# Optimization experiments

Measured on AMD Instinct MI355X. Metric: run time of the kernel, lower is better.

## Reference

```python
import jax, jax.numpy as jnp
import numpy as np

N = 100000
E = 1600000
C_IN = 128
C_OUT = 128
EPS = 1e-5


def setup_inputs() -> dict:
    key = jax.random.key(0)
    ks = jax.random.split(key, 8)
    x = jax.random.normal(ks[0], (N, C_IN), dtype=jnp.float32)
    edge_index = jax.random.randint(ks[1], (2, E), 0, N, dtype=jnp.int64)
    s_proj = 1.0 / np.sqrt(C_IN)
    s_out = 1.0 / np.sqrt(C_IN)
    W_proj = jax.random.uniform(ks[2], (C_IN, C_IN), jnp.float32, -s_proj, s_proj)
    b_proj = jax.random.uniform(ks[3], (C_IN,), jnp.float32, -s_proj, s_proj)
    W_l = jax.random.uniform(ks[4], (C_OUT, C_IN), jnp.float32, -s_out, s_out)
    b_l = jax.random.uniform(ks[5], (C_OUT,), jnp.float32, -s_out, s_out)
    W_r = jax.random.uniform(ks[6], (C_OUT, C_IN), jnp.float32, -s_out, s_out)
    gamma = jnp.ones((C_OUT,), jnp.float32)
    beta = jnp.zeros((C_OUT,), jnp.float32)
    return {"x": x, "edge_index": edge_index, "W_proj": W_proj, "b_proj": b_proj,
            "W_l": W_l, "b_l": b_l, "W_r": W_r, "gamma": gamma, "beta": beta}


def reference(x, edge_index, W_proj, b_proj, W_l, b_l, W_r, gamma, beta):
    # SAGEConv(project=True, aggr='sum'): project+ReLU source features per node,
    # gather along edges, scatter-sum at targets, then lin_l(agg) + lin_r(x_root).
    src, dst = edge_index[0], edge_index[1]
    h = jax.nn.relu(x @ W_proj.T + b_proj)            # [N, C_IN]
    msg = h[src]                                       # [E, C_IN] edge gather
    agg = jax.ops.segment_sum(msg, dst, num_segments=N)  # [N, C_IN]
    out = agg @ W_l.T + b_l + x @ W_r.T                # [N, C_OUT] (root uses unprojected x)
    # LayerNorm(c_out)
    mu = jnp.mean(out, axis=-1, keepdims=True)
    var = jnp.var(out, axis=-1, keepdims=True)
    return (out - mu) * jax.lax.rsqrt(var + EPS) * gamma + beta
```

## Files before the change

kernel.cpp:

```cpp
#include <hip/hip_runtime.h>
#include <stdint.h>

#define NN 100000
#define NE 1600000
#define C  128
#define NB 782
#define CAP 4096
#define SB_SHIFT 13
#define MB 782
#define P1B 250

typedef __attribute__((ext_vector_type(8))) short short8;
typedef __attribute__((ext_vector_type(4))) float f32x4;

__device__ __forceinline__ float bf2f(uint16_t u) {
  union { uint32_t u; float f; } v; v.u = ((uint32_t)u) << 16; return v.f;
}
__device__ __forceinline__ uint16_t f2bf(float f) {
  union { float f; uint32_t u; } v; v.f = f;
  uint32_t r = v.u + 0x7fffu + ((v.u >> 16) & 1u);
  return (uint16_t)(r >> 16);
}
__device__ __forceinline__ float2 bf2x2(uint32_t u) {
  return make_float2(bf2f((uint16_t)u), bf2f((uint16_t)(u >> 16)));
}

__global__ __launch_bounds__(256) void cast3_k(
    const float* __restrict__ a, const float* __restrict__ b, const float* __restrict__ c,
    uint16_t* __restrict__ oa, uint16_t* __restrict__ ob, uint16_t* __restrict__ oc)
{
  int i = blockIdx.x * 256 + threadIdx.x;
  int which = i >> 12, j = i & 4095;
  const float* s = which == 0 ? a : (which == 1 ? b : c);
  uint16_t* d    = which == 0 ? oa : (which == 1 ? ob : oc);
  float4 v = ((const float4*)s)[j];
  uint2 p;
  p.x = (uint32_t)f2bf(v.x) | ((uint32_t)f2bf(v.y) << 16);
  p.y = (uint32_t)f2bf(v.z) | ((uint32_t)f2bf(v.w) << 16);
  ((uint2*)d)[j] = p;
}


__global__ __launch_bounds__(512) void fused_front_k(
    const float* __restrict__ x, const uint16_t* __restrict__ wpb,
    const uint16_t* __restrict__ wrb,
    const float* __restrict__ bp, const float* __restrict__ bl,
    uint16_t* __restrict__ h, uint16_t* __restrict__ rb,
    const int* __restrict__ esrc, const int* __restrict__ edst,
    int* __restrict__ gcnt, uint32_t* __restrict__ ebuf)
{
  extern __shared__ uint8_t slds[];
  const int t = threadIdx.x;

  if (blockIdx.x < MB) {
#pragma unroll
    for (int qq = 0; qq < 4; ++qq) {
      int ci = qq * 512 + t;
      int c = ci >> 4, k16 = ci & 15;
      int slot = (k16 ^ (c & 15)) << 4;
      *(short8*)(slds + c * 256 + slot)         = *(const short8*)(wpb + ci * 8);
      *(short8*)(slds + 32768 + c * 256 + slot) = *(const short8*)(wrb + ci * 8);
    }
    __syncthreads();

    const int w = t >> 6, lane = t & 63;
    const int tile_m = blockIdx.x * 128 + w * 16;
    if (tile_m >= NN) return;
    const int r16 = lane & 15, g = lane >> 4;

    int arow = tile_m + r16; if (arow >= NN) arow = NN - 1;
    short8 a[4];
    const float* xp = x + (size_t)arow * C + g * 8;
#pragma unroll
    for (int kk = 0; kk < 4; ++kk) {
      float4 u = *(const float4*)(xp + kk * 32);
      float4 v = *(const float4*)(xp + kk * 32 + 4);
      short8 av;
      av[0] = (short)f2bf(u.x); av[1] = (short)f2bf(u.y);
      av[2] = (short)f2bf(u.z); av[3] = (short)f2bf(u.w);
      av[4] = (short)f2bf(v.x); av[5] = (short)f2bf(v.y);
      av[6] = (short)f2bf(v.z); av[7] = (short)f2bf(v.w);
      a[kk] = av;
    }

#pragma unroll
    for (int nt = 0; nt < 8; ++nt) {
      f32x4 ap = {0.f, 0.f, 0.f, 0.f};
      f32x4 ar = {0.f, 0.f, 0.f, 0.f};
      const int c = nt * 16 + r16;
      const uint8_t* rbp = slds + c * 256;
      const uint8_t* rbr = slds + 32768 + c * 256;
#pragma unroll
      for (int kk = 0; kk < 4; ++kk) {
        int slot = (((kk << 2) + g) ^ (c & 15)) << 4;
        ap = __builtin_amdgcn_mfma_f32_16x16x32_bf16(a[kk], *(const short8*)(rbp + slot), ap, 0, 0, 0);
        ar = __builtin_amdgcn_mfma_f32_16x16x32_bf16(a[kk], *(const short8*)(rbr + slot), ar, 0, 0, 0);
      }
      const float bpv = bp[c], blv = bl[c];
#pragma unroll
      for (int rr = 0; rr < 4; ++rr) {
        int row = tile_m + g * 4 + rr;
        if (row < NN) {
          float vh = ap[rr] + bpv;
          vh = vh > 0.f ? vh : 0.f;
          h[(size_t)row * C + c]  = f2bf(vh);
          rb[(size_t)row * C + c] = f2bf(ar[rr] + blv);
        }
      }
    }
  } else {
    int* bh = (int*)slds;
    int* gb = bh + NB;
    const int blk = blockIdx.x - MB;
    const int base = blk * 6400;

    for (int i = t; i < NB; i += 512) bh[i] = 0;

    const int4* ed4 = (const int4*)(edst + base);
    const int4* es4 = (const int4*)(esrc + base);
    int4 dv[4], sv[4];
    bool val[4];
#pragma unroll
    for (int k = 0; k < 4; ++k) {
      int i = t + k * 512;
      val[k] = (i < 1600);
      if (val[k]) { dv[k] = ed4[i]; sv[k] = es4[i]; }
    }
    __syncthreads();

#pragma unroll
    for (int k = 0; k < 4; ++k) if (val[k]) {
      atomicAdd(&bh[dv[k].x >> 7], 1); atomicAdd(&bh[dv[k].y >> 7], 1);
      atomicAdd(&bh[dv[k].z >> 7], 1); atomicAdd(&bh[dv[k].w >> 7], 1);
    }
    __syncthreads();

    for (int i = t; i < NB; i += 512) {
      int c = bh[i];
      gb[i] = c ? atomicAdd(&gcnt[i], c) : 0;
      bh[i] = 0;
    }
    __syncthreads();

#define P1_SCATTER(d, s) do { \
      int bb = (d) >> 7; \
      int o = atomicAdd(&bh[bb], 1); \
      int pos = gb[bb] + o; \
      if (pos < CAP) ebuf[(size_t)bb * CAP + pos] = ((uint32_t)((d) & 127) << 17) | (uint32_t)(s); \
    } while (0)

#pragma unroll
    for (int k = 0; k < 4; ++k) if (val[k]) {
      P1_SCATTER(dv[k].x, sv[k].x); P1_SCATTER(dv[k].y, sv[k].y);
      P1_SCATTER(dv[k].z, sv[k].z); P1_SCATTER(dv[k].w, sv[k].w);
    }
#undef P1_SCATTER
  }
}

__global__ __launch_bounds__(256) void phase2_k(
    const uint32_t* __restrict__ ebuf, const int* __restrict__ gcnt,
    int* __restrict__ ssrc, int2* __restrict__ sdeg)
{
  __shared__ uint32_t raw[CAP];
  __shared__ int lout[CAP];
  __shared__ int cnt2[128 * 16];
  __shared__ int nd[128];
  __shared__ int psum[256];
  const int b = blockIdx.x, t = threadIdx.x;
  const int n0 = b * 128;

  int acc = 0;
  for (int i = t; i < b; i += 256) acc += gcnt[i];
  psum[t] = acc;
  __syncthreads();
  for (int off = 128; off > 0; off >>= 1) {
    if (t < off) psum[t] += psum[t + off];
    __syncthreads();
  }
  const int base = psum[0];
  int cnt = gcnt[b]; if (cnt > CAP) cnt = CAP;

  for (int i = t; i < 128 * 16; i += 256) cnt2[i] = 0;
  __syncthreads();
  for (int i = t; i < cnt; i += 256) {
    uint32_t v = ebuf[(size_t)b * CAP + i];
    raw[i] = v;
    atomicAdd(&cnt2[(v >> 17) * 16 + ((v & 0x1FFFFu) >> SB_SHIFT)], 1);
  }
  __syncthreads();

  int deg_t = 0;
  if (t < 128) {
#pragma unroll
    for (int i = 0; i < 16; ++i) deg_t += cnt2[t * 16 + i];
    nd[t] = deg_t;
  }
  __syncthreads();
  for (int off = 1; off < 128; off <<= 1) {
    int v = 0;
    if (t < 128 && t >= off) v = nd[t - off];
    __syncthreads();
    if (t < 128) nd[t] += v;
    __syncthreads();
  }
  if (t < 128) {
    int pref = nd[t] - deg_t;
    if (n0 + t < NN) sdeg[n0 + t] = make_int2(base + pref, deg_t);
    int run = pref;
#pragma unroll
    for (int i = 0; i < 16; ++i) { int c = cnt2[t * 16 + i]; cnt2[t * 16 + i] = run; run += c; }
  }
  __syncthreads();
  for (int i = t; i < cnt; i += 256) {
    uint32_t v = raw[i];
    int o = atomicAdd(&cnt2[(v >> 17) * 16 + ((v & 0x1FFFFu) >> SB_SHIFT)], 1);
    lout[o] = (int)(v & 0x1FFFFu);
  }
  __syncthreads();
  for (int i = t; i < cnt; i += 256) ssrc[base + i] = lout[i];
}

__global__ __launch_bounds__(256) void aggregate_k(
    const uint16_t* __restrict__ h, const int* __restrict__ ssrc,
    const int2* __restrict__ sdeg, uint16_t* __restrict__ agg)
{
  const int wid = (blockIdx.x * 256 + threadIdx.x) >> 6;
  if (wid >= NN) return;
  const int lane = threadIdx.x & 63;
  const int q = lane >> 4;
  const int l16 = lane & 15;
  const int2 sd = sdeg[wid];
  const int s0 = sd.x, cnt = sd.y;
  const size_t choff = (size_t)l16 * 8;
  float2 a0 = {0.f, 0.f}, a1 = {0.f, 0.f}, a2 = {0.f, 0.f}, a3 = {0.f, 0.f};

#define ACC8(v) do { \
    a0 += bf2x2((v).x); a1 += bf2x2((v).y); \
    a2 += bf2x2((v).z); a3 += bf2x2((v).w); \
  } while (0)

  if (cnt > 0) {
    int e0 = ssrc[s0 + ((q      < cnt) ? q      : cnt - 1)];
    int e1 = ssrc[s0 + ((q + 4  < cnt) ? q + 4  : cnt - 1)];
    int e2 = ssrc[s0 + ((q + 8  < cnt) ? q + 8  : cnt - 1)];
    int e3 = ssrc[s0 + ((q + 12 < cnt) ? q + 12 : cnt - 1)];
    for (int j = 0; j < cnt; j += 16) {
      uint4 v0 = *(const uint4*)(h + (size_t)e0 * C + choff);
      uint4 v1 = *(const uint4*)(h + (size_t)e1 * C + choff);
      uint4 v2 = *(const uint4*)(h + (size_t)e2 * C + choff);
      uint4 v3 = *(const uint4*)(h + (size_t)e3 * C + choff);
      const int jn = j + 16;
      if (jn < cnt) {
        e0 = ssrc[s0 + ((jn + q      < cnt) ? jn + q      : cnt - 1)];
        e1 = ssrc[s0 + ((jn + q + 4  < cnt) ? jn + q + 4  : cnt - 1)];
        e2 = ssrc[s0 + ((jn + q + 8  < cnt) ? jn + q + 8  : cnt - 1)];
        e3 = ssrc[s0 + ((jn + q + 12 < cnt) ? jn + q + 12 : cnt - 1)];
      }
      if (j + q      < cnt) ACC8(v0);
      if (j + q + 4  < cnt) ACC8(v1);
      if (j + q + 8  < cnt) ACC8(v2);
      if (j + q + 12 < cnt) ACC8(v3);
    }
  }
#undef ACC8

#pragma unroll
  for (int msk = 16; msk <= 32; msk <<= 1) {
    a0.x += __shfl_xor(a0.x, msk, 64); a0.y += __shfl_xor(a0.y, msk, 64);
    a1.x += __shfl_xor(a1.x, msk, 64); a1.y += __shfl_xor(a1.y, msk, 64);
    a2.x += __shfl_xor(a2.x, msk, 64); a2.y += __shfl_xor(a2.y, msk, 64);
    a3.x += __shfl_xor(a3.x, msk, 64); a3.y += __shfl_xor(a3.y, msk, 64);
  }
  if (q == 0) {
    uint4 p;
    p.x = (uint32_t)f2bf(a0.x) | ((uint32_t)f2bf(a0.y) << 16);
    p.y = (uint32_t)f2bf(a1.x) | ((uint32_t)f2bf(a1.y) << 16);
    p.z = (uint32_t)f2bf(a2.x) | ((uint32_t)f2bf(a2.y) << 16);
    p.w = (uint32_t)f2bf(a3.x) | ((uint32_t)f2bf(a3.y) << 16);
    *(uint4*)(agg + (size_t)wid * C + choff) = p;
  }
}

__global__ __launch_bounds__(512) void gemm_out_k(
    const uint16_t* __restrict__ aggb, const uint16_t* __restrict__ rb,
    const uint16_t* __restrict__ wlb, const float* __restrict__ gamma,
    const float* __restrict__ beta, float* __restrict__ out)
{
  __shared__ uint8_t wl[32768];
  const int t = threadIdx.x;
#pragma unroll
  for (int qq = 0; qq < 4; ++qq) {
    int ci = qq * 512 + t;
    int c = ci >> 4, k16 = ci & 15;
    *(short8*)(wl + c * 256 + ((k16 ^ (c & 15)) << 4)) = *(const short8*)(wlb + ci * 8);
  }
  __syncthreads();

  const int w = t >> 6, lane = t & 63;
  const int tile_m = blockIdx.x * 128 + w * 16;
  if (tile_m >= NN) return;
  const int r16 = lane & 15, g = lane >> 4;

  int arow = tile_m + r16; if (arow >= NN) arow = NN - 1;
  short8 a0[4];
  const uint16_t* p0 = aggb + (size_t)arow * C + g * 8;
#pragma unroll
  for (int kk = 0; kk < 4; ++kk) a0[kk] = *(const short8*)(p0 + kk * 32);

  f32x4 acc[8];
#pragma unroll
  for (int nt = 0; nt < 8; ++nt) {
    f32x4 c4 = {0.f, 0.f, 0.f, 0.f};
    const int c = nt * 16 + r16;
    const uint8_t* rbl = wl + c * 256;
#pragma unroll
    for (int kk = 0; kk < 4; ++kk) {
      short8 b = *(const short8*)(rbl + ((((kk << 2) + g) ^ (c & 15)) << 4));
      c4 = __builtin_amdgcn_mfma_f32_16x16x32_bf16(a0[kk], b, c4, 0, 0, 0);
    }
#pragma unroll
    for (int rr = 0; rr < 4; ++rr) {
      int row = tile_m + g * 4 + rr;
      int crow = row < NN ? row : NN - 1;
      c4[rr] += bf2f(rb[(size_t)crow * C + c]);
    }
    acc[nt] = c4;
  }

  float s1[4], s2[4];
#pragma unroll
  for (int rr = 0; rr < 4; ++rr) { s1[rr] = 0.f; s2[rr] = 0.f; }
#pragma unroll
  for (int nt = 0; nt < 8; ++nt)
#pragma unroll
    for (int rr = 0; rr < 4; ++rr) { float v = acc[nt][rr]; s1[rr] += v; s2[rr] += v * v; }
#pragma unroll
  for (int msk = 1; msk <= 8; msk <<= 1) {
#pragma unroll
    for (int rr = 0; rr < 4; ++rr) {
      s1[rr] += __shfl_xor(s1[rr], msk, 64);
      s2[rr] += __shfl_xor(s2[rr], msk, 64);
    }
  }
  float mean[4], rstd[4];
#pragma unroll
  for (int rr = 0; rr < 4; ++rr) {
    mean[rr] = s1[rr] * (1.f / C);
    float var = s2[rr] * (1.f / C) - mean[rr] * mean[rr];
    rstd[rr] = rsqrtf(var + 1e-5f);
  }
#pragma unroll
  for (int nt = 0; nt < 8; ++nt) {
    const int col = nt * 16 + r16;
    const float gmv = gamma[col], btv = beta[col];
#pragma unroll
    for (int rr = 0; rr < 4; ++rr) {
      int row = tile_m + g * 4 + rr;
      if (row < NN)
        out[(size_t)row * C + col] = (acc[nt][rr] - mean[rr]) * rstd[rr] * gmv + btv;
    }
  }
}

extern "C" void kernel_launch(void* const* d_in, const int* in_sizes, int n_in,
                              void* d_out, int out_size, void* d_ws, size_t ws_size,
                              hipStream_t stream)
{
  const float* x        = (const float*)d_in[0];
  const int* ei         = (const int*)d_in[1];
  const float* Wp       = (const float*)d_in[2];
  const float* bp       = (const float*)d_in[3];
  const float* Wl       = (const float*)d_in[4];
  const float* bl       = (const float*)d_in[5];
  const float* Wr       = (const float*)d_in[6];
  const float* gamma    = (const float*)d_in[7];
  const float* beta     = (const float*)d_in[8];
  float* out            = (float*)d_out;

  char* ws = (char*)d_ws;
  uint16_t* rb   = (uint16_t*)(ws + 0);
  uint16_t* h    = (uint16_t*)(ws + 25600000);
  uint32_t* ebuf = (uint32_t*)(ws + 51200000);
  uint16_t* aggb = (uint16_t*)(ws + 51200000);
  uint16_t* wpb  = (uint16_t*)(ws + 76800000);
  uint16_t* wlb  = (uint16_t*)(ws + 76832768);
  uint16_t* wrb  = (uint16_t*)(ws + 76865536);
  int2* sdeg     = (int2*)(ws + 76898304);
  int* gcnt      = (int*)(ws + 77698304);
  int* ssrc      = (int*)(ws + 78102400);

  const int* esrc = ei;
  const int* edst = ei + NE;

  hipMemsetAsync(gcnt, 0, NB * sizeof(int), stream);

  cast3_k<<<48, 256, 0, stream>>>(Wp, Wl, Wr, wpb, wlb, wrb);

  fused_front_k<<<MB + P1B, 512, 65536, stream>>>(
      x, wpb, wrb, bp, bl, h, rb, esrc, edst, gcnt, ebuf);

  phase2_k<<<NB, 256, 0, stream>>>(ebuf, gcnt, ssrc, sdeg);

  aggregate_k<<<(NN + 3) / 4, 256, 0, stream>>>(h, ssrc, sdeg, aggb);

  gemm_out_k<<<MB, 512, 0, stream>>>(aggb, rb, wlb, gamma, beta, out);
}
```

Before: 141.1 us.

## Transpose MFMA operands for row-contiguous vector stores and double front-kernel block size

Both GEMM kernels swap the MFMA A/B operands so each lane holds four consecutive columns of one row. This turns scattered 2-byte stores and loads of h, rb and out into packed uint2/float4 row-contiguous accesses and makes the LayerNorm reduction a two-step shuffle across lane groups. The fused front kernel also moves to 1024-thread blocks, with half as many GEMM and edge-binning blocks each covering twice the work, which halves the per-block weight staging into LDS. The cost is lower occupancy per block and more work per edge-binning block.

```diff
diff --git a/kernel.cpp b/kernel.cpp
--- a/kernel.cpp
+++ b/kernel.cpp
@@ -7,8 +7,9 @@
 #define NB 782
 #define CAP 4096
 #define SB_SHIFT 13
-#define MB 782
-#define P1B 250
+#define MBF 391
+#define P1B 125
+#define MBO 782
 
 typedef __attribute__((ext_vector_type(8))) short short8;
 typedef __attribute__((ext_vector_type(4))) float f32x4;
@@ -41,7 +42,7 @@
 }
 
 
-__global__ __launch_bounds__(512) void fused_front_k(
+__global__ __launch_bounds__(1024) void fused_front_k(
     const float* __restrict__ x, const uint16_t* __restrict__ wpb,
     const uint16_t* __restrict__ wrb,
     const float* __restrict__ bp, const float* __restrict__ bl,
@@ -52,10 +53,10 @@
   extern __shared__ uint8_t slds[];
   const int t = threadIdx.x;
 
-  if (blockIdx.x < MB) {
-#pragma unroll
-    for (int qq = 0; qq < 4; ++qq) {
-      int ci = qq * 512 + t;
+  if (blockIdx.x < MBF) {
+#pragma unroll
+    for (int qq = 0; qq < 2; ++qq) {
+      int ci = qq * 1024 + t;
       int c = ci >> 4, k16 = ci & 15;
       int slot = (k16 ^ (c & 15)) << 4;
       *(short8*)(slds + c * 256 + slot)         = *(const short8*)(wpb + ci * 8);
@@ -64,11 +65,12 @@
     __syncthreads();
 
     const int w = t >> 6, lane = t & 63;
-    const int tile_m = blockIdx.x * 128 + w * 16;
+    const int tile_m = blockIdx.x * 256 + w * 16;
     if (tile_m >= NN) return;
     const int r16 = lane & 15, g = lane >> 4;
 
-    int arow = tile_m + r16; if (arow >= NN) arow = NN - 1;
+    const int row = tile_m + r16;
+    int arow = row < NN ? row : NN - 1;
     short8 a[4];
     const float* xp = x + (size_t)arow * C + g * 8;
 #pragma unroll
@@ -85,36 +87,41 @@
 
 #pragma unroll
     for (int nt = 0; nt < 8; ++nt) {
-      f32x4 ap = {0.f, 0.f, 0.f, 0.f};
-      f32x4 ar = {0.f, 0.f, 0.f, 0.f};
+      f32x4 hp = {0.f, 0.f, 0.f, 0.f};
+      f32x4 hr = {0.f, 0.f, 0.f, 0.f};
       const int c = nt * 16 + r16;
       const uint8_t* rbp = slds + c * 256;
       const uint8_t* rbr = slds + 32768 + c * 256;
 #pragma unroll
       for (int kk = 0; kk < 4; ++kk) {
         int slot = (((kk << 2) + g) ^ (c & 15)) << 4;
-        ap = __builtin_amdgcn_mfma_f32_16x16x32_bf16(a[kk], *(const short8*)(rbp + slot), ap, 0, 0, 0);
-        ar = __builtin_amdgcn_mfma_f32_16x16x32_bf16(a[kk], *(const short8*)(rbr + slot), ar, 0, 0, 0);
+        hp = __builtin_amdgcn_mfma_f32_16x16x32_bf16(*(const short8*)(rbp + slot), a[kk], hp, 0, 0, 0);
+        hr = __builtin_amdgcn_mfma_f32_16x16x32_bf16(*(const short8*)(rbr + slot), a[kk], hr, 0, 0, 0);
       }
-      const float bpv = bp[c], blv = bl[c];
-#pragma unroll
-      for (int rr = 0; rr < 4; ++rr) {
-        int row = tile_m + g * 4 + rr;
-        if (row < NN) {
-          float vh = ap[rr] + bpv;
-          vh = vh > 0.f ? vh : 0.f;
-          h[(size_t)row * C + c]  = f2bf(vh);
-          rb[(size_t)row * C + c] = f2bf(ar[rr] + blv);
-        }
+      const int col0 = nt * 16 + g * 4;
+      float4 bp4 = *(const float4*)(bp + col0);
+      float4 bl4 = *(const float4*)(bl + col0);
+      if (row < NN) {
+        float h0 = hp[0] + bp4.x, h1 = hp[1] + bp4.y, h2 = hp[2] + bp4.z, h3 = hp[3] + bp4.w;
+        h0 = h0 > 0.f ? h0 : 0.f; h1 = h1 > 0.f ? h1 : 0.f;
+        h2 = h2 > 0.f ? h2 : 0.f; h3 = h3 > 0.f ? h3 : 0.f;
+        uint2 ph;
+        ph.x = (uint32_t)f2bf(h0) | ((uint32_t)f2bf(h1) << 16);
+        ph.y = (uint32_t)f2bf(h2) | ((uint32_t)f2bf(h3) << 16);
+        *(uint2*)(h + (size_t)row * C + col0) = ph;
+        uint2 pr;
+        pr.x = (uint32_t)f2bf(hr[0] + bl4.x) | ((uint32_t)f2bf(hr[1] + bl4.y) << 16);
+        pr.y = (uint32_t)f2bf(hr[2] + bl4.z) | ((uint32_t)f2bf(hr[3] + bl4.w) << 16);
+        *(uint2*)(rb + (size_t)row * C + col0) = pr;
       }
     }
   } else {
     int* bh = (int*)slds;
     int* gb = bh + NB;
-    const int blk = blockIdx.x - MB;
-    const int base = blk * 6400;
-
-    for (int i = t; i < NB; i += 512) bh[i] = 0;
+    const int blk = blockIdx.x - MBF;
+    const int base = blk * 12800;
+
+    for (int i = t; i < NB; i += 1024) bh[i] = 0;
 
     const int4* ed4 = (const int4*)(edst + base);
     const int4* es4 = (const int4*)(esrc + base);
@@ -122,8 +129,8 @@
     bool val[4];
 #pragma unroll
     for (int k = 0; k < 4; ++k) {
-      int i = t + k * 512;
-      val[k] = (i < 1600);
+      int i = t + k * 1024;
+      val[k] = (i < 3200);
       if (val[k]) { dv[k] = ed4[i]; sv[k] = es4[i]; }
     }
     __syncthreads();
@@ -135,7 +142,7 @@
     }
     __syncthreads();
 
-    for (int i = t; i < NB; i += 512) {
+    for (int i = t; i < NB; i += 1024) {
       int c = bh[i];
       gb[i] = c ? atomicAdd(&gcnt[i], c) : 0;
       bh[i] = 0;
@@ -302,13 +309,15 @@
   if (tile_m >= NN) return;
   const int r16 = lane & 15, g = lane >> 4;
 
-  int arow = tile_m + r16; if (arow >= NN) arow = NN - 1;
+  const int row = tile_m + r16;
+  const int arow = row < NN ? row : NN - 1;
   short8 a0[4];
   const uint16_t* p0 = aggb + (size_t)arow * C + g * 8;
 #pragma unroll
   for (int kk = 0; kk < 4; ++kk) a0[kk] = *(const short8*)(p0 + kk * 32);
 
   f32x4 acc[8];
+  float s1 = 0.f, s2 = 0.f;
 #pragma unroll
   for (int nt = 0; nt < 8; ++nt) {
     f32x4 c4 = {0.f, 0.f, 0.f, 0.f};
@@ -317,48 +326,35 @@
 #pragma unroll
     for (int kk = 0; kk < 4; ++kk) {
       short8 b = *(const short8*)(rbl + ((((kk << 2) + g) ^ (c & 15)) << 4));
-      c4 = __builtin_amdgcn_mfma_f32_16x16x32_bf16(a0[kk], b, c4, 0, 0, 0);
-    }
-#pragma unroll
-    for (int rr = 0; rr < 4; ++rr) {
-      int row = tile_m + g * 4 + rr;
-      int crow = row < NN ? row : NN - 1;
-      c4[rr] += bf2f(rb[(size_t)crow * C + c]);
-    }
+      c4 = __builtin_amdgcn_mfma_f32_16x16x32_bf16(b, a0[kk], c4, 0, 0, 0);
+    }
+    const int col0 = nt * 16 + g * 4;
+    uint2 rv = *(const uint2*)(rb + (size_t)arow * C + col0);
+    float2 r01 = bf2x2(rv.x), r23 = bf2x2(rv.y);
+    c4[0] += r01.x; c4[1] += r01.y; c4[2] += r23.x; c4[3] += r23.y;
+#pragma unroll
+    for (int rr = 0; rr < 4; ++rr) { s1 += c4[rr]; s2 += c4[rr] * c4[rr]; }
     acc[nt] = c4;
   }
 
-  float s1[4], s2[4];
-#pragma unroll
-  for (int rr = 0; rr < 4; ++rr) { s1[rr] = 0.f; s2[rr] = 0.f; }
-#pragma unroll
-  for (int nt = 0; nt < 8; ++nt)
-#pragma unroll
-    for (int rr = 0; rr < 4; ++rr) { float v = acc[nt][rr]; s1[rr] += v; s2[rr] += v * v; }
-#pragma unroll
-  for (int msk = 1; msk <= 8; msk <<= 1) {
-#pragma unroll
-    for (int rr = 0; rr < 4; ++rr) {
-      s1[rr] += __shfl_xor(s1[rr], msk, 64);
-      s2[rr] += __shfl_xor(s2[rr], msk, 64);
-    }
-  }
-  float mean[4], rstd[4];
-#pragma unroll
-  for (int rr = 0; rr < 4; ++rr) {
-    mean[rr] = s1[rr] * (1.f / C);
-    float var = s2[rr] * (1.f / C) - mean[rr] * mean[rr];
-    rstd[rr] = rsqrtf(var + 1e-5f);
-  }
-#pragma unroll
-  for (int nt = 0; nt < 8; ++nt) {
-    const int col = nt * 16 + r16;
-    const float gmv = gamma[col], btv = beta[col];
-#pragma unroll
-    for (int rr = 0; rr < 4; ++rr) {
-      int row = tile_m + g * 4 + rr;
-      if (row < NN)
-        out[(size_t)row * C + col] = (acc[nt][rr] - mean[rr]) * rstd[rr] * gmv + btv;
+  s1 += __shfl_xor(s1, 16, 64); s2 += __shfl_xor(s2, 16, 64);
+  s1 += __shfl_xor(s1, 32, 64); s2 += __shfl_xor(s2, 32, 64);
+  const float mean = s1 * (1.f / C);
+  const float var = s2 * (1.f / C) - mean * mean;
+  const float rstd = rsqrtf(var + 1e-5f);
+
+  if (row < NN) {
+#pragma unroll
+    for (int nt = 0; nt < 8; ++nt) {
+      const int col0 = nt * 16 + g * 4;
+      float4 gm = *(const float4*)(gamma + col0);
+      float4 bt = *(const float4*)(beta + col0);
+      float4 o;
+      o.x = (acc[nt][0] - mean) * rstd * gm.x + bt.x;
+      o.y = (acc[nt][1] - mean) * rstd * gm.y + bt.y;
+      o.z = (acc[nt][2] - mean) * rstd * gm.z + bt.z;
+      o.w = (acc[nt][3] - mean) * rstd * gm.w + bt.w;
+      *(float4*)(out + (size_t)row * C + col0) = o;
     }
   }
 }
@@ -397,12 +393,12 @@
 
   cast3_k<<<48, 256, 0, stream>>>(Wp, Wl, Wr, wpb, wlb, wrb);
 
-  fused_front_k<<<MB + P1B, 512, 65536, stream>>>(
+  fused_front_k<<<MBF + P1B, 1024, 65536, stream>>>(
       x, wpb, wrb, bp, bl, h, rb, esrc, edst, gcnt, ebuf);
 
   phase2_k<<<NB, 256, 0, stream>>>(ebuf, gcnt, ssrc, sdeg);
 
   aggregate_k<<<(NN + 3) / 4, 256, 0, stream>>>(h, ssrc, sdeg, aggb);
 
-  gemm_out_k<<<MB, 512, 0, stream>>>(aggb, rb, wlb, gamma, beta, out);
-}
+  gemm_out_k<<<MBO, 512, 0, stream>>>(aggb, rb, wlb, gamma, beta, out);
+}
```

New measurement: 150.8 us. 6.8% more time.
